# Optimization experiments

Measured on AMD Instinct MI355X. Metric: run time of the kernel, lower is better.

## Reference

```python
import jax, jax.numpy as jnp
import numpy as np

N_HEADS = 32
N_KV = 8
GROUPS = 4
D_HEAD = 64
ROPE_BASE = 10000.0


def _rope_tables(seq_len):
    # inv_freq over even dims, emb = [freqs, freqs] along last axis (torch cat([outer]*2))
    inv_freq = 1.0 / (ROPE_BASE ** (jnp.arange(0, D_HEAD, 2, dtype=jnp.float32) / D_HEAD))
    t = jnp.arange(seq_len, dtype=jnp.float32)
    freqs = jnp.outer(t, inv_freq)                      # [S, D_HEAD/2]
    emb = jnp.concatenate([freqs, freqs], axis=-1)      # [S, D_HEAD]
    return jnp.cos(emb), jnp.sin(emb)


def _rotate_half(x):
    h = x.shape[-1] // 2
    return jnp.concatenate([-x[..., h:], x[..., :h]], axis=-1)


def setup_inputs() -> dict:
    key = jax.random.key(0)
    ks = jax.random.split(key, 5)
    B, S, D = 4, 2048, 2048
    s = 0.02
    return {
        "x": jax.random.normal(ks[0], (B, S, D), dtype=jnp.float32),
        "Wq": jax.random.normal(ks[1], (D, D), dtype=jnp.float32) * s,
        "Wk": jax.random.normal(ks[2], (N_KV * D_HEAD, D), dtype=jnp.float32) * s,
        "Wv": jax.random.normal(ks[3], (N_KV * D_HEAD, D), dtype=jnp.float32) * s,
        "Wo": jax.random.normal(ks[4], (D, D), dtype=jnp.float32) * s,
        "temperature": jnp.float32(1.0),
    }


def reference(x, Wq, Wk, Wv, Wo, temperature):
    B, S, D = x.shape
    # QKV projections (torch Linear: x @ W.T)
    Q = jnp.einsum('bsd,ed->bse', x, Wq).reshape(B, S, N_HEADS, D_HEAD).transpose(0, 2, 1, 3)
    K = jnp.einsum('bsd,ed->bse', x, Wk).reshape(B, S, N_KV, D_HEAD).transpose(0, 2, 1, 3)
    V = jnp.einsum('bsd,ed->bse', x, Wv).reshape(B, S, N_KV, D_HEAD).transpose(0, 2, 1, 3)

    # RoPE (offset=0, no past_kv)
    cos, sin = _rope_tables(S)          # [S, D_HEAD]
    cos = cos[None, None]
    sin = sin[None, None]
    Q = Q * cos + _rotate_half(Q) * sin
    K = K * cos + _rotate_half(K) * sin

    kv_cache = (K, V)  # pre-expansion cache, as in original

    # GQA expand: each kv head repeated GROUPS times along head axis
    Ke = jnp.repeat(K, GROUPS, axis=1)  # [B, N_HEADS, S, D_HEAD]
    Ve = jnp.repeat(V, GROUPS, axis=1)

    # scale uses .item() in torch -> constant w.r.t. autograd
    scale = (D_HEAD ** -0.5) / jnp.maximum(jnp.abs(temperature), 1e-6)
    scale = jax.lax.stop_gradient(scale)

    scores = jnp.einsum('bhqd,bhkd->bhqk', Q, Ke) * scale
    causal = jnp.tril(jnp.ones((S, S), dtype=bool))
    scores = jnp.where(causal[None, None], scores, jnp.finfo(scores.dtype).min)
    attn = jax.nn.softmax(scores, axis=-1)
    out = jnp.einsum('bhqk,bhkd->bhqd', attn, Ve)       # [B, H, S, D_HEAD]

    out = out.transpose(0, 2, 1, 3).reshape(B, S, D)
    y = jnp.einsum('bsd,ed->bse', out, Wo)
    return (y, kv_cache[0], kv_cache[1])
```

## Files before the change

### kernel.cpp

```cpp
#include <hip/hip_runtime.h>

#define S_LEN  2048
#define DMODEL 2048
#define NH     32
#define NKV    8
#define DH     64

typedef _Float16 h8   __attribute__((ext_vector_type(8)));
typedef _Float16 h4   __attribute__((ext_vector_type(4)));
typedef float    f32x4 __attribute__((ext_vector_type(4)));

__device__ __forceinline__ void load_lds16(const _Float16* g, _Float16* l) {
  typedef const __attribute__((address_space(1))) unsigned int* gp_t;
  typedef __attribute__((address_space(3))) unsigned int* lp_t;
  __builtin_amdgcn_global_load_lds((gp_t)g, (lp_t)l, 16, 0, 0);
}

#define N8_X  2097152
#define N8_WQ 524288
#define N8_WK 131072
#define N8_WV 131072
#define N8_WO 524288
#define N8_ALL (N8_X + N8_WQ + N8_WK + N8_WV + N8_WO)
__global__ void cvt_all(const float* __restrict__ x, const float* __restrict__ wq,
                        const float* __restrict__ wk, const float* __restrict__ wv,
                        const float* __restrict__ wo, _Float16* __restrict__ dst) {
  int stride = gridDim.x * blockDim.x;
  for (int i = blockIdx.x * blockDim.x + threadIdx.x; i < N8_ALL; i += stride) {
    const float* s;
    int off;
    if (i < N8_X) { s = x; off = i; }
    else if (i < N8_X + N8_WQ) { s = wq; off = i - N8_X; }
    else if (i < N8_X + N8_WQ + N8_WK) { s = wk; off = i - (N8_X + N8_WQ); }
    else if (i < N8_X + N8_WQ + N8_WK + N8_WV) { s = wv; off = i - (N8_X + N8_WQ + N8_WK); }
    else { s = wo; off = i - (N8_X + N8_WQ + N8_WK + N8_WV); }
    float4 a = ((const float4*)s)[2 * off];
    float4 b = ((const float4*)s)[2 * off + 1];
    h8 v = {(_Float16)a.x, (_Float16)a.y, (_Float16)a.z, (_Float16)a.w,
            (_Float16)b.x, (_Float16)b.y, (_Float16)b.z, (_Float16)b.w};
    ((h8*)dst)[i] = v;
  }
}

__global__ void rope_table_k(float2* __restrict__ tab) {
  int i = blockIdx.x * blockDim.x + threadIdx.x;
  int s = i >> 5, d = i & 31;
  float invf = (float)exp2(-(double)d * 0.4152410118609203);
  float angf = (float)s * invf;
  double a = (double)angf;
  const double twopi = 6.283185307179586476925287;
  a -= floor(a / twopi) * twopi;
  tab[i] = make_float2((float)cos(a), (float)sin(a));
}

template <int MODE>
__global__ __launch_bounds__(512) void gemm128(
    const _Float16* __restrict__ A, const _Float16* __restrict__ Bm,
    _Float16* __restrict__ qH, _Float16* __restrict__ kH, float* __restrict__ kF,
    _Float16* __restrict__ vH, float* __restrict__ vF, float* __restrict__ yF,
    const float2* __restrict__ rtab, const float* __restrict__ tptr) {
  __shared__ __align__(16) _Float16 lA[2][128 * 32];
  __shared__ __align__(16) _Float16 lB[2][128 * 32];
  const int Kd = 2048;
  int t = threadIdx.x;
  int w = t >> 6, lane = t & 63;
  int n0 = blockIdx.x * 128, m0 = blockIdx.y * 128;
  int wr = w >> 1, wc = w & 1;
  int lq = lane & 15, hi = lane >> 4;

  const _Float16* gA = A + (size_t)(m0 + w * 16 + (lane >> 2)) * Kd + (lane & 3) * 8;
  const _Float16* gB = Bm + (size_t)(n0 + w * 16 + (lane >> 2)) * Kd + (lane & 3) * 8;
  int dOff = (w * 16) * 32;

  f32x4 z4 = {0.f, 0.f, 0.f, 0.f};
  f32x4 acc[2][4];
#pragma unroll
  for (int i = 0; i < 2; i++)
#pragma unroll
    for (int j = 0; j < 4; j++) acc[i][j] = z4;

  load_lds16(gA, &lA[0][dOff]);
  load_lds16(gB, &lB[0][dOff]);
  asm volatile("s_waitcnt vmcnt(0)" ::: "memory");
  __builtin_amdgcn_s_barrier();

  for (int k0 = 0; k0 < Kd; k0 += 32) {
    int cur = (k0 >> 5) & 1;
    if (k0 + 32 < Kd) {
      load_lds16(gA + k0 + 32, &lA[cur ^ 1][dOff]);
      load_lds16(gB + k0 + 32, &lB[cur ^ 1][dOff]);
    }
    h8 af[2], bf[4];
#pragma unroll
    for (int i = 0; i < 2; i++)
      af[i] = *(const h8*)&lA[cur][(wr * 32 + i * 16 + lq) * 32 + hi * 8];
#pragma unroll
    for (int j = 0; j < 4; j++)
      bf[j] = *(const h8*)&lB[cur][(wc * 64 + j * 16 + lq) * 32 + hi * 8];
#pragma unroll
    for (int i = 0; i < 2; i++)
#pragma unroll
      for (int j = 0; j < 4; j++)
        acc[i][j] = __builtin_amdgcn_mfma_f32_16x16x32_f16(af[i], bf[j], acc[i][j], 0, 0, 0);
    asm volatile("s_waitcnt vmcnt(0)" ::: "memory");
    __builtin_amdgcn_s_barrier();
  }

  if (MODE == 3) {
#pragma unroll
    for (int ci = 0; ci < 4; ci++) {
      int col = n0 + wc * 64 + ci * 16 + lq;
#pragma unroll
      for (int mi = 0; mi < 2; mi++)
#pragma unroll
        for (int r = 0; r < 4; r++) {
          int m = m0 + wr * 32 + mi * 16 + hi * 4 + r;
          yF[(size_t)m * DMODEL + col] = acc[mi][ci][r];
        }
    }
  } else {
    int base64 = n0 + wc * 64;
    if (base64 < 2048) {
      float qsc = 0.125f / fmaxf(fabsf(tptr[0]), 1e-6f) * 1.4426950408889634f;
      int head = base64 >> 6;
#pragma unroll
      for (int ci = 0; ci < 2; ci++) {
        int dlo = ci * 16 + lq;
#pragma unroll
        for (int mi = 0; mi < 2; mi++)
#pragma unroll
          for (int r = 0; r < 4; r++) {
            int m = m0 + wr * 32 + mi * 16 + hi * 4 + r;
            int b = m >> 11, s = m & 2047;
            float2 cs = rtab[s * 32 + dlo];
            float lo = acc[mi][ci][r], hv = acc[mi][ci + 2][r];
            float olo = (lo * cs.x - hv * cs.y) * qsc;
            float ohi = (hv * cs.x + lo * cs.y) * qsc;
            size_t base = ((size_t)(b * NH + head) * S_LEN + s) * DH;
            qH[base + dlo] = (_Float16)olo;
            qH[base + dlo + 32] = (_Float16)ohi;
          }
      }
    } else if (base64 < 2560) {
      int head = (base64 - 2048) >> 6;
#pragma unroll
      for (int ci = 0; ci < 2; ci++) {
        int dlo = ci * 16 + lq;
#pragma unroll
        for (int mi = 0; mi < 2; mi++)
#pragma unroll
          for (int r = 0; r < 4; r++) {
            int m = m0 + wr * 32 + mi * 16 + hi * 4 + r;
            int b = m >> 11, s = m & 2047;
            float2 cs = rtab[s * 32 + dlo];
            float lo = acc[mi][ci][r], hv = acc[mi][ci + 2][r];
            float olo = lo * cs.x - hv * cs.y;
            float ohi = hv * cs.x + lo * cs.y;
            size_t bb = ((size_t)(b * NKV + head) * S_LEN + s) * DH;
            kH[bb + dlo] = (_Float16)olo;
            kH[bb + dlo + 32] = (_Float16)ohi;
            kF[bb + dlo] = olo;
            kF[bb + dlo + 32] = ohi;
          }
      }
    } else {
      int head = (base64 - 2560) >> 6;
#pragma unroll
      for (int ci = 0; ci < 4; ci++) {
        int d = ci * 16 + lq;
#pragma unroll
        for (int mi = 0; mi < 2; mi++)
#pragma unroll
          for (int r = 0; r < 4; r++) {
            int m = m0 + wr * 32 + mi * 16 + hi * 4 + r;
            int b = m >> 11, s = m & 2047;
            float v = acc[mi][ci][r];
            vH[((size_t)(b * NKV + head) * DH + d) * S_LEN + s] = (_Float16)v;
            vF[((size_t)(b * NKV + head) * S_LEN + s) * DH + d] = v;
          }
      }
    }
  }
}

__global__ __launch_bounds__(256, 3) void attn_fwd(
    const _Float16* __restrict__ Q, const _Float16* __restrict__ K,
    const _Float16* __restrict__ Vt, _Float16* __restrict__ AO) {
  __shared__ __align__(16) _Float16 lP[4][32 * 72];
  __shared__ __align__(16) _Float16 lK[2][64 * 64];
  __shared__ __align__(16) _Float16 lV[2][64 * 64];
  int t = threadIdx.x, w = t >> 6, lane = t & 63;
  int lq = lane & 15, hi = lane >> 4;

  int bh = blockIdx.x * 16 + (blockIdx.y & 15);
  int qb = 15 - (blockIdx.y >> 4);
  int b = bh >> 5, h = bh & 31, g = h >> 2;

  const _Float16* Qp = Q + ((size_t)(b * NH + h) * S_LEN) * DH;
  const _Float16* Kp = K + ((size_t)(b * NKV + g) * S_LEN) * DH;
  const _Float16* Vp = Vt + ((size_t)(b * NKV + g) * DH) * S_LEN;

  f32x4 z4 = {0.f, 0.f, 0.f, 0.f};
  int q0 = qb * 128 + w * 32;

  int swz = ((lane & 7) ^ (lane >> 3)) * 8;
  size_t sko0 = (size_t)(w * 16 + (lane >> 3)) * DH + (size_t)swz;
  size_t svo0 = (size_t)(w * 16 + (lane >> 3)) * S_LEN + (size_t)swz;

  h8 qf[2][2];
#pragma unroll
  for (int cf = 0; cf < 2; cf++)
#pragma unroll
    for (int dc = 0; dc < 2; dc++)
      qf[cf][dc] = *(const h8*)&Qp[(size_t)(q0 + lq + 16 * cf) * DH + dc * 32 + hi * 8];

  f32x4 ot[4][2];
#pragma unroll
  for (int rf = 0; rf < 4; rf++)
#pragma unroll
    for (int cf = 0; cf < 2; cf++) ot[rf][cf] = z4;
  float mrun[2] = {-3e38f, -3e38f};
  float lrun[2] = {0.f, 0.f};

  int NT = 2 * qb + 2;

  load_lds16(Kp + sko0, &lK[0][(w * 16) * 64]);
  load_lds16(Kp + sko0 + (size_t)8 * DH, &lK[0][(w * 16 + 8) * 64]);
  load_lds16(Vp + svo0, &lV[0][(w * 16) * 64]);
  load_lds16(Vp + svo0 + (size_t)8 * S_LEN, &lV[0][(w * 16 + 8) * 64]);

  for (int tk = 0; tk < NT; tk++) {
    int kv0 = tk * 64;

    asm volatile("s_waitcnt vmcnt(0)" ::: "memory");
    __builtin_amdgcn_s_barrier();

    if (tk + 1 < NT) {
      _Float16* nK = &lK[(tk + 1) & 1][0];
      _Float16* nV = &lV[(tk + 1) & 1][0];
      size_t kvn = (size_t)(kv0 + 64);
      load_lds16(Kp + kvn * DH + sko0, nK + (w * 16) * 64);
      load_lds16(Kp + kvn * DH + sko0 + (size_t)8 * DH, nK + (w * 16 + 8) * 64);
      load_lds16(Vp + svo0 + kvn, nV + (w * 16) * 64);
      load_lds16(Vp + svo0 + kvn + (size_t)8 * S_LEN, nV + (w * 16 + 8) * 64);
    }

    f32x4 sc[4][2];
#pragma unroll
    for (int rf = 0; rf < 4; rf++)
#pragma unroll
      for (int cf = 0; cf < 2; cf++) sc[rf][cf] = z4;
    {
      const _Float16* kb = &lK[tk & 1][0];
#pragma unroll
      for (int dc = 0; dc < 2; dc++) {
        h8 kf[4];
#pragma unroll
        for (int rf = 0; rf < 4; rf++)
          kf[rf] = *(const h8*)&kb[(rf * 16 + lq) * 64 + (((dc * 4 + hi) ^ (lq & 7)) * 8)];
#pragma unroll
        for (int rf = 0; rf < 4; rf++)
#pragma unroll
          for (int cf = 0; cf < 2; cf++)
            sc[rf][cf] = __builtin_amdgcn_mfma_f32_16x16x32_f16(kf[rf], qf[cf][dc], sc[rf][cf], 0, 0, 0);
      }
    }

    if (kv0 + 63 > q0) {
#pragma unroll
      for (int rf = 0; rf < 4; rf++)
#pragma unroll
        for (int cf = 0; cf < 2; cf++)
#pragma unroll
          for (int r = 0; r < 4; r++) {
            int kv = kv0 + rf * 16 + hi * 4 + r;
            int q = q0 + lq + 16 * cf;
            if (kv > q) sc[rf][cf][r] = -1e30f;
          }
    }

    float mt[2];
#pragma unroll
    for (int cf = 0; cf < 2; cf++) {
      float m2 = -3e38f;
#pragma unroll
      for (int rf = 0; rf < 4; rf++)
#pragma unroll
        for (int r = 0; r < 4; r++) m2 = fmaxf(m2, sc[rf][cf][r]);
      m2 = fmaxf(m2, __shfl_xor(m2, 16));
      m2 = fmaxf(m2, __shfl_xor(m2, 32));
      mt[cf] = m2;
    }

    bool need = !__all((mt[0] - mrun[0] <= 8.f) && (mt[1] - mrun[1] <= 8.f));
    if (need) {
#pragma unroll
      for (int cf = 0; cf < 2; cf++) {
        float mnew = fmaxf(mrun[cf], mt[cf]);
        float al = __builtin_amdgcn_exp2f(mrun[cf] - mnew);
        mrun[cf] = mnew;
        lrun[cf] *= al;
#pragma unroll
        for (int rf = 0; rf < 4; rf++)
#pragma unroll
          for (int r = 0; r < 4; r++) ot[rf][cf][r] *= al;
      }
    }

    float ls[2] = {0.f, 0.f};
#pragma unroll
    for (int rf = 0; rf < 4; rf++)
#pragma unroll
      for (int cf = 0; cf < 2; cf++)
#pragma unroll
        for (int r = 0; r < 4; r++) {
          float p = __builtin_amdgcn_exp2f(sc[rf][cf][r] - mrun[cf]);
          sc[rf][cf][r] = p;
          ls[cf] += p;
        }
#pragma unroll
    for (int cf = 0; cf < 2; cf++) {
      float s2 = ls[cf];
      s2 += __shfl_xor(s2, 16);
      s2 += __shfl_xor(s2, 32);
      lrun[cf] += s2;
    }

#pragma unroll
    for (int rf = 0; rf < 4; rf++)
#pragma unroll
      for (int cf = 0; cf < 2; cf++) {
        h4 p4;
#pragma unroll
        for (int r = 0; r < 4; r++) p4[r] = (_Float16)sc[rf][cf][r];
        *(h4*)&lP[w][(lq + 16 * cf) * 72 + rf * 16 + hi * 4] = p4;
      }
    asm volatile("s_waitcnt lgkmcnt(0)" ::: "memory");
    __builtin_amdgcn_sched_barrier(0);

    {
      const _Float16* vb = &lV[tk & 1][0];
#pragma unroll
      for (int kvc = 0; kvc < 2; kvc++) {
        h8 vf[4];
#pragma unroll
        for (int rf = 0; rf < 4; rf++)
          vf[rf] = *(const h8*)&vb[(rf * 16 + lq) * 64 + (((kvc * 4 + hi) ^ (lq & 7)) * 8)];
        h8 pb[2];
#pragma unroll
        for (int cf = 0; cf < 2; cf++)
          pb[cf] = *(const h8*)&lP[w][(lq + 16 * cf) * 72 + kvc * 32 + hi * 8];
#pragma unroll
        for (int rf = 0; rf < 4; rf++)
#pragma unroll
          for (int cf = 0; cf < 2; cf++)
            ot[rf][cf] = __builtin_amdgcn_mfma_f32_16x16x32_f16(vf[rf], pb[cf], ot[rf][cf], 0, 0, 0);
      }
    }
  }

#pragma unroll
  for (int cf = 0; cf < 2; cf++) {
    float inv = 1.0f / lrun[cf];
    size_t row = (size_t)b * S_LEN + q0 + lq + 16 * cf;
#pragma unroll
    for (int rf = 0; rf < 4; rf++) {
      h4 o;
#pragma unroll
      for (int r = 0; r < 4; r++) o[r] = (_Float16)(ot[rf][cf][r] * inv);
      *(h4*)&AO[row * DMODEL + h * DH + rf * 16 + hi * 4] = o;
    }
  }
}

extern "C" void kernel_launch(void* const* d_in, const int* in_sizes, int n_in,
                              void* d_out, int out_size, void* d_ws, size_t ws_size,
                              hipStream_t stream) {
  const float* x  = (const float*)d_in[0];
  const float* Wq = (const float*)d_in[1];
  const float* Wk = (const float*)d_in[2];
  const float* Wv = (const float*)d_in[3];
  const float* Wo = (const float*)d_in[4];
  const float* tp = (const float*)d_in[5];

  float* y  = (float*)d_out;
  float* Ko = y + (size_t)16777216;
  float* Vo = Ko + (size_t)4194304;

  _Float16* xh  = (_Float16*)d_ws;
  _Float16* wqh = xh + 16777216;
  _Float16* wkh = wqh + 4194304;
  _Float16* wvh = wkh + 1048576;
  _Float16* woh = wvh + 1048576;
  _Float16* Kh  = woh + 4194304;
  _Float16* Vth = Kh + 4194304;
  float2*   rtab = (float2*)(Vth + 4194304);
  _Float16* AOh = xh;
  _Float16* Qh  = (_Float16*)d_out;
  (void)wkh; (void)wvh;

  cvt_all<<<2048, 256, 0, stream>>>(x, Wq, Wk, Wv, Wo, xh);
  rope_table_k<<<256, 256, 0, stream>>>(rtab);

  gemm128<1><<<dim3(24, 64), 512, 0, stream>>>(xh, wqh, Qh, Kh, Ko, Vth, Vo, nullptr, rtab, tp);
  attn_fwd<<<dim3(8, 256), 256, 0, stream>>>(Qh, Kh, Vth, AOh);
  gemm128<3><<<dim3(16, 64), 512, 0, stream>>>(AOh, woh, nullptr, nullptr, nullptr, nullptr, nullptr, y, rtab, tp);
}
```

Measured before the change: 396.7 us.

## Enlarge GEMM tiles to 256x256x64 with swizzled LDS and deeper prefetch

Replaces the 128x128x32 projection GEMM with a 256x256 output tile over a K step of 64, so each wave computes a 128x64 sub-tile. LDS rows are XOR-swizzled to avoid bank conflicts, and partial vmcnt waits let the next tile's loads overlap compute. MFMA bursts are wrapped in s_setprio. This raises data reuse per LDS load but uses 128 KB of LDS and many accumulator registers, which limits occupancy and leaves a partial last wave for the QKV grid.

```diff
diff --git a/kernel.cpp b/kernel.cpp
--- a/kernel.cpp
+++ b/kernel.cpp
@@ -54,56 +54,88 @@
 }
 
 template <int MODE>
-__global__ __launch_bounds__(512) void gemm128(
+__global__ __launch_bounds__(512, 2) void gemm256(
     const _Float16* __restrict__ A, const _Float16* __restrict__ Bm,
     _Float16* __restrict__ qH, _Float16* __restrict__ kH, float* __restrict__ kF,
     _Float16* __restrict__ vH, float* __restrict__ vF, float* __restrict__ yF,
     const float2* __restrict__ rtab, const float* __restrict__ tptr) {
-  __shared__ __align__(16) _Float16 lA[2][128 * 32];
-  __shared__ __align__(16) _Float16 lB[2][128 * 32];
+  __shared__ __align__(16) _Float16 lA[2][256 * 64];
+  __shared__ __align__(16) _Float16 lB[2][256 * 64];
   const int Kd = 2048;
   int t = threadIdx.x;
   int w = t >> 6, lane = t & 63;
-  int n0 = blockIdx.x * 128, m0 = blockIdx.y * 128;
-  int wr = w >> 1, wc = w & 1;
+  int n0 = blockIdx.x * 256, m0 = blockIdx.y * 256;
+  int wr = w >> 2, wc = w & 3;
   int lq = lane & 15, hi = lane >> 4;
 
-  const _Float16* gA = A + (size_t)(m0 + w * 16 + (lane >> 2)) * Kd + (lane & 3) * 8;
-  const _Float16* gB = Bm + (size_t)(n0 + w * 16 + (lane >> 2)) * Kd + (lane & 3) * 8;
-  int dOff = (w * 16) * 32;
+  int swz = ((lane & 7) ^ (lane >> 3)) * 8;
+  const _Float16* pA = A + (size_t)(m0 + w * 32 + (lane >> 3)) * Kd + swz;
+  const _Float16* pB = Bm + (size_t)(n0 + w * 32 + (lane >> 3)) * Kd + swz;
+  int dRow = (w * 32) * 64;
 
   f32x4 z4 = {0.f, 0.f, 0.f, 0.f};
-  f32x4 acc[2][4];
-#pragma unroll
-  for (int i = 0; i < 2; i++)
+  f32x4 acc[8][4];
+#pragma unroll
+  for (int i = 0; i < 8; i++)
 #pragma unroll
     for (int j = 0; j < 4; j++) acc[i][j] = z4;
 
-  load_lds16(gA, &lA[0][dOff]);
-  load_lds16(gB, &lB[0][dOff]);
-  asm volatile("s_waitcnt vmcnt(0)" ::: "memory");
-  __builtin_amdgcn_s_barrier();
-
-  for (int k0 = 0; k0 < Kd; k0 += 32) {
-    int cur = (k0 >> 5) & 1;
-    if (k0 + 32 < Kd) {
-      load_lds16(gA + k0 + 32, &lA[cur ^ 1][dOff]);
-      load_lds16(gB + k0 + 32, &lB[cur ^ 1][dOff]);
-    }
-    h8 af[2], bf[4];
-#pragma unroll
-    for (int i = 0; i < 2; i++)
-      af[i] = *(const h8*)&lA[cur][(wr * 32 + i * 16 + lq) * 32 + hi * 8];
+#pragma unroll
+  for (int i = 0; i < 4; i++)
+    load_lds16(pB + (size_t)(i * 8) * Kd, &lB[0][dRow + i * 8 * 64]);
+#pragma unroll
+  for (int i = 0; i < 4; i++)
+    load_lds16(pA + (size_t)(i * 8) * Kd, &lA[0][dRow + i * 8 * 64]);
+
+  const int NT = Kd / 64;
+  for (int tt = 0; tt < NT; tt++) {
+    int cur = tt & 1, nxt = cur ^ 1;
+
+    asm volatile("s_waitcnt vmcnt(4)" ::: "memory");
+    __builtin_amdgcn_s_barrier();
+
+    if (tt + 1 < NT) {
+      int k0n = (tt + 1) * 64;
+#pragma unroll
+      for (int i = 0; i < 4; i++)
+        load_lds16(pB + (size_t)(i * 8) * Kd + k0n, &lB[nxt][dRow + i * 8 * 64]);
+#pragma unroll
+      for (int i = 0; i < 4; i++)
+        load_lds16(pA + (size_t)(i * 8) * Kd + k0n, &lA[nxt][dRow + i * 8 * 64]);
+    }
+
+    h8 bf[4][2];
 #pragma unroll
     for (int j = 0; j < 4; j++)
-      bf[j] = *(const h8*)&lB[cur][(wc * 64 + j * 16 + lq) * 32 + hi * 8];
-#pragma unroll
-    for (int i = 0; i < 2; i++)
-#pragma unroll
-      for (int j = 0; j < 4; j++)
-        acc[i][j] = __builtin_amdgcn_mfma_f32_16x16x32_f16(af[i], bf[j], acc[i][j], 0, 0, 0);
-    asm volatile("s_waitcnt vmcnt(0)" ::: "memory");
+#pragma unroll
+      for (int s = 0; s < 2; s++)
+        bf[j][s] = *(const h8*)&lB[cur][(wc * 64 + j * 16 + lq) * 64 + (((s * 4 + hi) ^ (lq & 7)) * 8)];
+
+    if (tt + 1 < NT) {
+      asm volatile("s_waitcnt vmcnt(8)" ::: "memory");
+    } else {
+      asm volatile("s_waitcnt vmcnt(0)" ::: "memory");
+    }
     __builtin_amdgcn_s_barrier();
+
+#pragma unroll
+    for (int p = 0; p < 4; p++) {
+      h8 af[2][2];
+#pragma unroll
+      for (int di = 0; di < 2; di++)
+#pragma unroll
+        for (int s = 0; s < 2; s++)
+          af[di][s] = *(const h8*)&lA[cur][(wr * 128 + (p * 2 + di) * 16 + lq) * 64 + (((s * 4 + hi) ^ (lq & 7)) * 8)];
+      __builtin_amdgcn_s_setprio(1);
+#pragma unroll
+      for (int s = 0; s < 2; s++)
+#pragma unroll
+        for (int di = 0; di < 2; di++)
+#pragma unroll
+          for (int j = 0; j < 4; j++)
+            acc[p * 2 + di][j] = __builtin_amdgcn_mfma_f32_16x16x32_f16(af[di][s], bf[j][s], acc[p * 2 + di][j], 0, 0, 0);
+      __builtin_amdgcn_s_setprio(0);
+    }
   }
 
   if (MODE == 3) {
@@ -111,11 +143,11 @@
     for (int ci = 0; ci < 4; ci++) {
       int col = n0 + wc * 64 + ci * 16 + lq;
 #pragma unroll
-      for (int mi = 0; mi < 2; mi++)
+      for (int i = 0; i < 8; i++)
 #pragma unroll
         for (int r = 0; r < 4; r++) {
-          int m = m0 + wr * 32 + mi * 16 + hi * 4 + r;
-          yF[(size_t)m * DMODEL + col] = acc[mi][ci][r];
+          int m = m0 + wr * 128 + i * 16 + hi * 4 + r;
+          yF[(size_t)m * DMODEL + col] = acc[i][ci][r];
         }
     }
   } else {
@@ -127,13 +159,13 @@
       for (int ci = 0; ci < 2; ci++) {
         int dlo = ci * 16 + lq;
 #pragma unroll
-        for (int mi = 0; mi < 2; mi++)
+        for (int i = 0; i < 8; i++)
 #pragma unroll
           for (int r = 0; r < 4; r++) {
-            int m = m0 + wr * 32 + mi * 16 + hi * 4 + r;
+            int m = m0 + wr * 128 + i * 16 + hi * 4 + r;
             int b = m >> 11, s = m & 2047;
             float2 cs = rtab[s * 32 + dlo];
-            float lo = acc[mi][ci][r], hv = acc[mi][ci + 2][r];
+            float lo = acc[i][ci][r], hv = acc[i][ci + 2][r];
             float olo = (lo * cs.x - hv * cs.y) * qsc;
             float ohi = (hv * cs.x + lo * cs.y) * qsc;
             size_t base = ((size_t)(b * NH + head) * S_LEN + s) * DH;
@@ -147,13 +179,13 @@
       for (int ci = 0; ci < 2; ci++) {
         int dlo = ci * 16 + lq;
 #pragma unroll
-        for (int mi = 0; mi < 2; mi++)
+        for (int i = 0; i < 8; i++)
 #pragma unroll
           for (int r = 0; r < 4; r++) {
-            int m = m0 + wr * 32 + mi * 16 + hi * 4 + r;
+            int m = m0 + wr * 128 + i * 16 + hi * 4 + r;
             int b = m >> 11, s = m & 2047;
             float2 cs = rtab[s * 32 + dlo];
-            float lo = acc[mi][ci][r], hv = acc[mi][ci + 2][r];
+            float lo = acc[i][ci][r], hv = acc[i][ci + 2][r];
             float olo = lo * cs.x - hv * cs.y;
             float ohi = hv * cs.x + lo * cs.y;
             size_t bb = ((size_t)(b * NKV + head) * S_LEN + s) * DH;
@@ -169,12 +201,12 @@
       for (int ci = 0; ci < 4; ci++) {
         int d = ci * 16 + lq;
 #pragma unroll
-        for (int mi = 0; mi < 2; mi++)
+        for (int i = 0; i < 8; i++)
 #pragma unroll
           for (int r = 0; r < 4; r++) {
-            int m = m0 + wr * 32 + mi * 16 + hi * 4 + r;
+            int m = m0 + wr * 128 + i * 16 + hi * 4 + r;
             int b = m >> 11, s = m & 2047;
-            float v = acc[mi][ci][r];
+            float v = acc[i][ci][r];
             vH[((size_t)(b * NKV + head) * DH + d) * S_LEN + s] = (_Float16)v;
             vF[((size_t)(b * NKV + head) * S_LEN + s) * DH + d] = v;
           }
@@ -402,7 +434,7 @@
   cvt_all<<<2048, 256, 0, stream>>>(x, Wq, Wk, Wv, Wo, xh);
   rope_table_k<<<256, 256, 0, stream>>>(rtab);
 
-  gemm128<1><<<dim3(24, 64), 512, 0, stream>>>(xh, wqh, Qh, Kh, Ko, Vth, Vo, nullptr, rtab, tp);
+  gemm256<1><<<dim3(12, 32), 512, 0, stream>>>(xh, wqh, Qh, Kh, Ko, Vth, Vo, nullptr, rtab, tp);
   attn_fwd<<<dim3(8, 256), 256, 0, stream>>>(Qh, Kh, Vth, AOh);
-  gemm128<3><<<dim3(16, 64), 512, 0, stream>>>(AOh, woh, nullptr, nullptr, nullptr, nullptr, nullptr, y, rtab, tp);
-}
+  gemm256<3><<<dim3(8, 32), 512, 0, stream>>>(AOh, woh, nullptr, nullptr, nullptr, nullptr, nullptr, y, rtab, tp);
+}
```

Result: faster. 367.4 us (-7.4%).
